# Kernel tuning notes

Hardware: AMD Instinct MI355X
Metric: run time of the kernel (lower is better)

The kernel has to match this reference:

```python
import jax, jax.numpy as jnp
import numpy as np

N = 50000
E = 800000
IN_DIM = 128
HEADS = 4
OUT_DIM = 32
TOT = HEADS * OUT_DIM  # 128 == IN_DIM -> residual_proj is None
LN_EPS = 1e-5
NEG_SLOPE = 0.2


def setup_inputs() -> dict:
    key = jax.random.key(0)
    ks = jax.random.split(key, 10)
    x = jax.random.normal(ks[0], (N, IN_DIM), dtype=jnp.float32)
    # random edges guaranteed src != dst (PyG GATv2Conv removes then re-adds self loops)
    src = jax.random.randint(ks[1], (E,), 0, N)
    off = jax.random.randint(ks[2], (E,), 1, N)
    dst = (src + off) % N
    edge_index = jnp.stack([src, dst]).astype(jnp.int64)
    # glorot-style init for weights
    sc = 1.0 / np.sqrt(IN_DIM)
    W_l = jax.random.uniform(ks[3], (IN_DIM, TOT), jnp.float32, -sc, sc)
    b_l = jnp.zeros((TOT,), jnp.float32)
    W_r = jax.random.uniform(ks[4], (IN_DIM, TOT), jnp.float32, -sc, sc)
    b_r = jnp.zeros((TOT,), jnp.float32)
    att = jax.random.uniform(ks[5], (HEADS, OUT_DIM), jnp.float32, -sc, sc)
    bias = jnp.zeros((TOT,), jnp.float32)
    ln_g = jnp.ones((TOT,), jnp.float32)
    ln_b = jnp.zeros((TOT,), jnp.float32)
    return {"x": x, "edge_index": edge_index, "W_l": W_l, "b_l": b_l,
            "W_r": W_r, "b_r": b_r, "att": att, "bias": bias,
            "ln_g": ln_g, "ln_b": ln_b}


def _gatv2_layer(x, src, dst, W_l, b_l, W_r, b_r, att, bias, ln_g, ln_b):
    n = x.shape[0]
    # GATv2Conv: x_l = lin_l(x) (source/messages), x_r = lin_r(x) (target)
    xl = (x @ W_l + b_l).reshape(n, HEADS, OUT_DIM)
    xr = (x @ W_r + b_r).reshape(n, HEADS, OUT_DIM)
    m = xl[src] + xr[dst]                               # [E+N, H, D]
    s = jnp.einsum('ehd,hd->eh', jax.nn.leaky_relu(m, NEG_SLOPE), att)
    # per-destination softmax (every node has a self loop -> no empty segments)
    smax = jax.ops.segment_max(s, dst, num_segments=n)  # [N, H]
    e = jnp.exp(s - smax[dst])
    denom = jax.ops.segment_sum(e, dst, num_segments=n)
    alpha = e / denom[dst]                              # [E+N, H]
    out = jax.ops.segment_sum(alpha[..., None] * xl[src], dst, num_segments=n)
    out = out.reshape(n, TOT) + bias
    out = out + x                                       # residual (in_dim == total_out_dim)
    mu = jnp.mean(out, axis=-1, keepdims=True)
    var = jnp.mean(jnp.square(out - mu), axis=-1, keepdims=True)
    y = (out - mu) / jnp.sqrt(var + LN_EPS) * ln_g + ln_b
    return jax.nn.elu(y)


def reference(x, edge_index, W_l, b_l, W_r, b_r, att, bias, ln_g, ln_b):
    n = x.shape[0]
    loops = jnp.arange(n, dtype=edge_index.dtype)
    src = jnp.concatenate([edge_index[0], loops])
    dst = jnp.concatenate([edge_index[1], loops])
    return _gatv2_layer(x, src, dst, W_l, b_l, W_r, b_r, att, bias, ln_g, ln_b)
```

## Files before the change

### kernel.cpp

```cpp
#include <hip/hip_runtime.h>

#define N_NODES 50000
#define E_EDGES 800000
#define M_TOTAL (E_EDGES + N_NODES)
#define IN_DIM 128
#define HEADS 4
#define OUT_DIM 32
#define TOT 128
#define LN_EPS 1e-5f
#define NEG_SLOPE 0.2f
#define LOG2E 1.4426950408889634f

#define SCAN_NBLK ((N_NODES + 255) / 256)
#define GEMM_NBLK ((N_NODES + 63) / 64)
#define HIST_NBLK 128
#define EPB 6656
#define HEPB (EPB / 2)
#define SCAT_NBLK (HIST_NBLK * 2)

typedef __bf16 bf16x8 __attribute__((ext_vector_type(8)));
typedef float  f32x4  __attribute__((ext_vector_type(4)));
typedef _Float16 h2   __attribute__((ext_vector_type(2)));

__device__ __forceinline__ float quad_sum(float p) {
    p += __int_as_float(__builtin_amdgcn_update_dpp(
        0, __float_as_int(p), 0xB1 , 0xF, 0xF, true));
    p += __int_as_float(__builtin_amdgcn_update_dpp(
        0, __float_as_int(p), 0x4E , 0xF, 0xF, true));
    return p;
}

__global__ __launch_bounds__(256) void wthist_kernel(
    const int* __restrict__ dsts,
    const float* __restrict__ Wl, const float* __restrict__ Wr,
    unsigned* __restrict__ WT, unsigned char* __restrict__ HP,
    unsigned char* __restrict__ rank8) {
    __shared__ unsigned cnt[N_NODES / 4];
    const int b = blockIdx.x, t = threadIdx.x;
    if (b < 64) {
        const int u = b * 256 + t;
        const int col = u >> 6, k2 = u & 63;
        const float* __restrict__ W = (col < 128) ? Wl : Wr;
        const int c = col & 127;
        union { __bf16 bb[2]; unsigned uu; } p;
        p.bb[0] = (__bf16)W[(2 * k2) * TOT + c];
        p.bb[1] = (__bf16)W[(2 * k2 + 1) * TOT + c];
        WT[col * 64 + k2] = p.uu;
        return;
    }
    const int hb = b - 64;
    const int m_begin = hb * EPB;
    const int m_end = min(m_begin + EPB, M_TOTAL);
    for (int i = t; i < N_NODES / 4; i += 256) cnt[i] = 0;
    __syncthreads();
    for (int m0 = m_begin + t * 4; m0 < m_end; m0 += 1024) {
        int d[4];
        if (m0 < E_EDGES) {
            const int4 dv = *(const int4*)&dsts[m0];
            d[0] = dv.x; d[1] = dv.y; d[2] = dv.z; d[3] = dv.w;
        } else {
            d[0] = m0 - E_EDGES; d[1] = d[0] + 1; d[2] = d[0] + 2; d[3] = d[0] + 3;
        }
        uchar4 r;
        unsigned old, sh;
        sh = (d[0] & 3) * 8; old = atomicAdd(&cnt[d[0] >> 2], 1u << sh);
        r.x = (unsigned char)(old >> sh);
        sh = (d[1] & 3) * 8; old = atomicAdd(&cnt[d[1] >> 2], 1u << sh);
        r.y = (unsigned char)(old >> sh);
        sh = (d[2] & 3) * 8; old = atomicAdd(&cnt[d[2] >> 2], 1u << sh);
        r.z = (unsigned char)(old >> sh);
        sh = (d[3] & 3) * 8; old = atomicAdd(&cnt[d[3] >> 2], 1u << sh);
        r.w = (unsigned char)(old >> sh);
        *(uchar4*)&rank8[m0] = r;
    }
    __syncthreads();
    unsigned* __restrict__ Hrow = (unsigned*)(HP + (size_t)hb * N_NODES);
    for (int i = t; i < N_NODES / 4; i += 256) Hrow[i] = cnt[i];
}

__global__ __launch_bounds__(256) void scan1gemm_kernel(
    unsigned char* __restrict__ HP,
    int* __restrict__ incl, int* __restrict__ blockSums,
    int* __restrict__ degtot,
    const float* __restrict__ x, const unsigned* __restrict__ WT,
    const float* __restrict__ bl, const float* __restrict__ br,
    unsigned* __restrict__ xlb, unsigned* __restrict__ xrb) {
    __shared__ float epi[4][16][66];
    const int t = threadIdx.x;
    if (blockIdx.x >= GEMM_NBLK) {
        int* sh = (int*)epi;
        const int i = (blockIdx.x - GEMM_NBLK) * 256 + t;
        int tot = 0;
        if (i < N_NODES) {
            int run = 0;
#pragma unroll 16
            for (int b = 0; b < HIST_NBLK; ++b) {
                const int h = HP[(size_t)b * N_NODES + i];
                HP[(size_t)b * N_NODES + i] = (unsigned char)run;
                run += h;
            }
            tot = run;
            degtot[i] = tot;
        }
        sh[t] = tot;
        __syncthreads();
#pragma unroll
        for (int off = 1; off < 256; off <<= 1) {
            int u = (t >= off) ? sh[t - off] : 0;
            __syncthreads();
            sh[t] += u;
            __syncthreads();
        }
        if (i < N_NODES) incl[i] = sh[t];
        if (t == 255) blockSums[blockIdx.x - GEMM_NBLK] = sh[255];
        return;
    }
    const int w = t >> 6, lane = t & 63;
    const int q = lane >> 4, ln = lane & 15;
    const int m0 = blockIdx.x * 64;

    const int row = min(m0 + w * 16 + ln, N_NODES - 1);
    const float* __restrict__ xrow = x + (size_t)row * IN_DIM;
    bf16x8 A[4];
#pragma unroll
    for (int c = 0; c < 4; ++c) {
        const float4 v0 = *(const float4*)&xrow[c * 32 + q * 8];
        const float4 v1 = *(const float4*)&xrow[c * 32 + q * 8 + 4];
        bf16x8 a;
        a[0] = (__bf16)v0.x; a[1] = (__bf16)v0.y; a[2] = (__bf16)v0.z; a[3] = (__bf16)v0.w;
        a[4] = (__bf16)v1.x; a[5] = (__bf16)v1.y; a[6] = (__bf16)v1.z; a[7] = (__bf16)v1.w;
        A[c] = a;
    }

    const int mr = lane >> 2, cg2 = (lane & 3) * 16;
    const int grow = m0 + w * 16 + mr;
#pragma unroll
    for (int g = 0; g < 4; ++g) {
        const int n0 = g * 64;
        const float* __restrict__ bvec = (g < 2) ? bl : br;
        f32x4 acc[4];
#pragma unroll
        for (int nt = 0; nt < 4; ++nt) {
            const float b = bvec[(n0 & 127) + nt * 16 + ln];
            acc[nt] = (f32x4){b, b, b, b};
        }
#pragma unroll
        for (int nt = 0; nt < 4; ++nt) {
            const int col = n0 + nt * 16 + ln;
#pragma unroll
            for (int c = 0; c < 4; ++c) {
                const bf16x8 B = *(const bf16x8*)&WT[col * 64 + c * 16 + q * 4];
                acc[nt] = __builtin_amdgcn_mfma_f32_16x16x32_bf16(A[c], B, acc[nt], 0, 0, 0);
            }
        }
#pragma unroll
        for (int nt = 0; nt < 4; ++nt)
#pragma unroll
            for (int r = 0; r < 4; ++r)
                epi[w][q * 4 + r][nt * 16 + ln] = acc[nt][r];

        if (grow < N_NODES) {
            unsigned p[8];
#pragma unroll
            for (int i = 0; i < 8; ++i) {
                union { _Float16 h[2]; unsigned u; } pk;
                pk.h[0] = (_Float16)epi[w][mr][cg2 + 2 * i];
                pk.h[1] = (_Float16)epi[w][mr][cg2 + 2 * i + 1];
                p[i] = pk.u;
            }
            unsigned* __restrict__ dst = ((g < 2) ? xlb : xrb) +
                (size_t)grow * 64 + (g & 1) * 32 + (cg2 >> 1);
            *(uint4*)&dst[0] = make_uint4(p[0], p[1], p[2], p[3]);
            *(uint4*)&dst[4] = make_uint4(p[4], p[5], p[6], p[7]);
        }
    }
}

__global__ __launch_bounds__(256) void scan23_kernel(
    const int* __restrict__ degtot, const int* __restrict__ blockSums,
    int* __restrict__ rowptr ,
    unsigned short* __restrict__ sorted16) {
    __shared__ int sh[256];
    const int t = threadIdx.x;
    const int v0 = (t < SCAN_NBLK) ? blockSums[t] : 0;
    sh[t] = v0;
    __syncthreads();
#pragma unroll
    for (int off = 1; off < 256; off <<= 1) {
        int u = (t >= off) ? sh[t - off] : 0;
        __syncthreads();
        sh[t] += u;
        __syncthreads();
    }
    const int blockOff = (blockIdx.x == 0) ? 0 : sh[blockIdx.x - 1];
    const int i = blockIdx.x * 256 + t;
    if (i < N_NODES)
        rowptr[i] = blockOff + rowptr[i] - degtot[i];
    if (i == 0) rowptr[N_NODES] = M_TOTAL;
    if (blockIdx.x == 0 && t < 32) sorted16[M_TOTAL + t] = 0;
}

__global__ __launch_bounds__(512) void scatter_kernel(
    const int* __restrict__ srcs, const int* __restrict__ dsts,
    const int* __restrict__ rowptr, const unsigned char* __restrict__ P,
    const unsigned char* __restrict__ rank8,
    unsigned short* __restrict__ sorted16) {
    __shared__ __align__(16) unsigned char smem[N_NODES];
    const int t = threadIdx.x;
    const int sb = blockIdx.x;
    const int hb = sb >> 1;
    const uint4* __restrict__ Prow = (const uint4*)(P + (size_t)hb * N_NODES);
    for (int i = t; i < N_NODES / 16; i += 512)
        ((uint4*)smem)[i] = Prow[i];
    __syncthreads();
    const int eb = hb * EPB + (sb & 1) * HEPB;
    const int ee = min(eb + HEPB, M_TOTAL);
    for (int m0 = eb + t * 4; m0 < ee; m0 += 2048) {
        int s[4], d[4];
        if (m0 < E_EDGES) {
            const int4 sv = *(const int4*)&srcs[m0];
            const int4 dv = *(const int4*)&dsts[m0];
            s[0] = sv.x; s[1] = sv.y; s[2] = sv.z; s[3] = sv.w;
            d[0] = dv.x; d[1] = dv.y; d[2] = dv.z; d[3] = dv.w;
        } else {
            s[0] = d[0] = m0 - E_EDGES;
            s[1] = d[1] = d[0] + 1; s[2] = d[2] = d[0] + 2; s[3] = d[3] = d[0] + 3;
        }
        const uchar4 r = *(const uchar4*)&rank8[m0];
        sorted16[rowptr[d[0]] + (int)smem[d[0]] + (int)r.x] = (unsigned short)s[0];
        sorted16[rowptr[d[1]] + (int)smem[d[1]] + (int)r.y] = (unsigned short)s[1];
        sorted16[rowptr[d[2]] + (int)smem[d[2]] + (int)r.z] = (unsigned short)s[2];
        sorted16[rowptr[d[3]] + (int)smem[d[3]] + (int)r.w] = (unsigned short)s[3];
    }
}

__global__ __launch_bounds__(256) void gat_kernel(
    const int* __restrict__ rowptr, const unsigned short* __restrict__ sorted16,
    const unsigned* __restrict__ xlb, const unsigned* __restrict__ xrb,
    const float* __restrict__ att, const float* __restrict__ x,
    const float* __restrict__ bias, const float* __restrict__ g,
    const float* __restrict__ bvec, float* __restrict__ out) {
    const int d = blockIdx.x * 4 + (threadIdx.x >> 6);
    const int lane = threadIdx.x & 63;
    const int ln = lane & 15, q = lane >> 4;
    if (d >= N_NODES) return;

    h2 xrh[4], ath[4];
    {
        const uint4 ur = *(const uint4*)&xrb[(size_t)d * 64 + 4 * ln];
        union { uint4 u; h2 h[4]; } cr; cr.u = ur;
        xrh[0] = cr.h[0]; xrh[1] = cr.h[1]; xrh[2] = cr.h[2]; xrh[3] = cr.h[3];
        const float4 a0 = *(const float4*)&att[8 * ln];
        const float4 a1 = *(const float4*)&att[8 * ln + 4];
        ath[0][0] = (_Float16)(a0.x * LOG2E); ath[0][1] = (_Float16)(a0.y * LOG2E);
        ath[1][0] = (_Float16)(a0.z * LOG2E); ath[1][1] = (_Float16)(a0.w * LOG2E);
        ath[2][0] = (_Float16)(a1.x * LOG2E); ath[2][1] = (_Float16)(a1.y * LOG2E);
        ath[3][0] = (_Float16)(a1.z * LOG2E); ath[3][1] = (_Float16)(a1.w * LOG2E);
    }
    const h2 slope = (h2){(_Float16)NEG_SLOPE, (_Float16)NEG_SLOPE};
    const int beg = rowptr[d], end = rowptr[d + 1];

    float l = 0.f;
    h2 acc4[4];
#pragma unroll
    for (int k = 0; k < 4; ++k) acc4[k] = (h2){(_Float16)0.f, (_Float16)0.f};

    uint4 u0, u1;
    {
        const int sA0 = (int)sorted16[beg + q];
        const int sA1 = (int)sorted16[beg + 4 + q];
        u0 = *(const uint4*)&xlb[(size_t)sA0 * 64 + 4 * ln];
        u1 = *(const uint4*)&xlb[(size_t)sA1 * 64 + 4 * ln];
    }
    int sB0 = (int)sorted16[beg + 8 + q];
    int sB1 = (int)sorted16[beg + 12 + q];

    for (int base = beg; base < end; base += 8) {
        const int sC0 = (int)sorted16[base + 16 + q];
        const int sC1 = (int)sorted16[base + 20 + q];
        const uint4 un0 = *(const uint4*)&xlb[(size_t)sB0 * 64 + 4 * ln];
        const uint4 un1 = *(const uint4*)&xlb[(size_t)sB1 * 64 + 4 * ln];

        union { unsigned uu; h2 h; } a0, a1, a2, a3, b0, b1, b2, b3;
        a0.uu = u0.x; a1.uu = u0.y; a2.uu = u0.z; a3.uu = u0.w;
        b0.uu = u1.x; b1.uu = u1.y; b2.uu = u1.z; b3.uu = u1.w;
        h2 mA0 = a0.h + xrh[0], mA1 = a1.h + xrh[1];
        h2 mA2 = a2.h + xrh[2], mA3 = a3.h + xrh[3];
        h2 mB0 = b0.h + xrh[0], mB1 = b1.h + xrh[1];
        h2 mB2 = b2.h + xrh[2], mB3 = b3.h + xrh[3];
        mA0 = __builtin_elementwise_max(mA0, mA0 * slope);
        mA1 = __builtin_elementwise_max(mA1, mA1 * slope);
        mA2 = __builtin_elementwise_max(mA2, mA2 * slope);
        mA3 = __builtin_elementwise_max(mA3, mA3 * slope);
        mB0 = __builtin_elementwise_max(mB0, mB0 * slope);
        mB1 = __builtin_elementwise_max(mB1, mB1 * slope);
        mB2 = __builtin_elementwise_max(mB2, mB2 * slope);
        mB3 = __builtin_elementwise_max(mB3, mB3 * slope);
        float p0 = __builtin_amdgcn_fdot2(mA0, ath[0], 0.0f, false);
        p0 = __builtin_amdgcn_fdot2(mA1, ath[1], p0, false);
        p0 = __builtin_amdgcn_fdot2(mA2, ath[2], p0, false);
        p0 = __builtin_amdgcn_fdot2(mA3, ath[3], p0, false);
        float p1 = __builtin_amdgcn_fdot2(mB0, ath[0], 0.0f, false);
        p1 = __builtin_amdgcn_fdot2(mB1, ath[1], p1, false);
        p1 = __builtin_amdgcn_fdot2(mB2, ath[2], p1, false);
        p1 = __builtin_amdgcn_fdot2(mB3, ath[3], p1, false);
        p0 = quad_sum(p0);
        p1 = quad_sum(p1);
        const float e0 = (base + q < end) ? exp2f(p0) : 0.f;
        const float e1 = (base + 4 + q < end) ? exp2f(p1) : 0.f;
        l += e0 + e1;
        const _Float16 eh0 = (_Float16)e0, eh1 = (_Float16)e1;
        const h2 e20 = (h2){eh0, eh0}, e21 = (h2){eh1, eh1};
        acc4[0] += e20 * a0.h; acc4[0] += e21 * b0.h;
        acc4[1] += e20 * a1.h; acc4[1] += e21 * b1.h;
        acc4[2] += e20 * a2.h; acc4[2] += e21 * b2.h;
        acc4[3] += e20 * a3.h; acc4[3] += e21 * b3.h;

        u0 = un0; u1 = un1; sB0 = sC0; sB1 = sC1;
    }

#pragma unroll
    for (int off = 16; off <= 32; off <<= 1) {
        l += __shfl_xor(l, off, 64);
#pragma unroll
        for (int k = 0; k < 4; ++k) {
            union { h2 h; int i; } tmp; tmp.h = acc4[k];
            tmp.i = __shfl_xor(tmp.i, off, 64);
            acc4[k] += tmp.h;
        }
    }
    float acc[8];
#pragma unroll
    for (int k = 0; k < 4; ++k) {
        acc[2 * k]     = (float)acc4[k][0];
        acc[2 * k + 1] = (float)acc4[k][1];
    }

    const float inv_l = 1.0f / l;
    const float4 xv0 = *(const float4*)&x[(size_t)d * TOT + 8 * ln];
    const float4 xv1 = *(const float4*)&x[(size_t)d * TOT + 8 * ln + 4];
    const float4 bi0 = *(const float4*)&bias[8 * ln];
    const float4 bi1 = *(const float4*)&bias[8 * ln + 4];
    float v[8];
    v[0] = fmaf(acc[0], inv_l, bi0.x + xv0.x);
    v[1] = fmaf(acc[1], inv_l, bi0.y + xv0.y);
    v[2] = fmaf(acc[2], inv_l, bi0.z + xv0.z);
    v[3] = fmaf(acc[3], inv_l, bi0.w + xv0.w);
    v[4] = fmaf(acc[4], inv_l, bi1.x + xv1.x);
    v[5] = fmaf(acc[5], inv_l, bi1.y + xv1.y);
    v[6] = fmaf(acc[6], inv_l, bi1.z + xv1.z);
    v[7] = fmaf(acc[7], inv_l, bi1.w + xv1.w);
    float sum = 0.f, sq = 0.f;
#pragma unroll
    for (int k = 0; k < 8; ++k) { sum += v[k]; sq = fmaf(v[k], v[k], sq); }
#pragma unroll
    for (int off = 1; off <= 8; off <<= 1) {
        sum += __shfl_xor(sum, off, 64);
        sq  += __shfl_xor(sq,  off, 64);
    }
    const float mu  = sum * (1.0f / TOT);
    const float var = sq * (1.0f / TOT) - mu * mu;
    const float inv = rsqrtf(var + LN_EPS);
    const float4 g0 = *(const float4*)&g[8 * ln];
    const float4 g1 = *(const float4*)&g[8 * ln + 4];
    const float4 b0 = *(const float4*)&bvec[8 * ln];
    const float4 b1 = *(const float4*)&bvec[8 * ln + 4];
    float y[8];
    y[0] = (v[0] - mu) * inv * g0.x + b0.x;
    y[1] = (v[1] - mu) * inv * g0.y + b0.y;
    y[2] = (v[2] - mu) * inv * g0.z + b0.z;
    y[3] = (v[3] - mu) * inv * g0.w + b0.w;
    y[4] = (v[4] - mu) * inv * g1.x + b1.x;
    y[5] = (v[5] - mu) * inv * g1.y + b1.y;
    y[6] = (v[6] - mu) * inv * g1.z + b1.z;
    y[7] = (v[7] - mu) * inv * g1.w + b1.w;
#pragma unroll
    for (int k = 0; k < 8; ++k) y[k] = y[k] > 0.f ? y[k] : __expf(y[k]) - 1.f;
    if (q < 2) {
        float4 o = (q == 0) ? make_float4(y[0], y[1], y[2], y[3])
                            : make_float4(y[4], y[5], y[6], y[7]);
        *(float4*)&out[(size_t)d * TOT + 8 * ln + 4 * q] = o;
    }
}

extern "C" void kernel_launch(void* const* d_in, const int* in_sizes, int n_in,
                              void* d_out, int out_size, void* d_ws, size_t ws_size,
                              hipStream_t stream) {
    const float* x    = (const float*)d_in[0];
    const int*   ei   = (const int*)d_in[1];
    const float* Wl   = (const float*)d_in[2];
    const float* bl   = (const float*)d_in[3];
    const float* Wr   = (const float*)d_in[4];
    const float* br   = (const float*)d_in[5];
    const float* att  = (const float*)d_in[6];
    const float* bias = (const float*)d_in[7];
    const float* ln_g = (const float*)d_in[8];
    const float* ln_b = (const float*)d_in[9];
    const int* srcs = ei;
    const int* dsts = ei + E_EDGES;

    unsigned* xlb = (unsigned*)d_ws;
    unsigned* xrb = xlb + (size_t)N_NODES * 64;
    int*   degtot     = (int*)(xrb + (size_t)N_NODES * 64);
    int*   rowptr     = degtot + N_NODES;
    int*   blockSums  = rowptr + N_NODES + 1;
    unsigned* WT      = (unsigned*)(blockSums + SCAN_NBLK + 3);
    unsigned char* HP = (unsigned char*)(WT + 256 * 64);
    unsigned short* sorted16 = (unsigned short*)(HP + (size_t)HIST_NBLK * N_NODES);
    unsigned char*  rank8    = (unsigned char*)(sorted16 + M_TOTAL + 32);

    wthist_kernel<<<64 + HIST_NBLK, 256, 0, stream>>>(dsts, Wl, Wr, WT, HP, rank8);
    scan1gemm_kernel<<<GEMM_NBLK + SCAN_NBLK, 256, 0, stream>>>(
        HP, rowptr, blockSums, degtot, x, WT, bl, br, xlb, xrb);
    scan23_kernel<<<SCAN_NBLK, 256, 0, stream>>>(degtot, blockSums, rowptr, sorted16);
    scatter_kernel<<<SCAT_NBLK, 512, 0, stream>>>(srcs, dsts, rowptr, HP, rank8, sorted16);
    gat_kernel<<<(N_NODES + 3) / 4, 256, 0, stream>>>(rowptr, sorted16, xlb, xrb, att, x,
                                                      bias, ln_g, ln_b, (float*)d_out);
}
```

Measured before the change: 188.6 us.

## Split GEMM and scan kernels, stage weights in LDS, widen scatter blocks

The fused scan/GEMM kernel is split into separate GEMM and scan1 launches. The GEMM now stages each 64-column weight slice in shared memory before the MFMA loop instead of reading it from global memory per lane. The scatter kernel goes from two 512-thread blocks per histogram row to one 1024-thread block, so each histogram row is loaded into LDS once rather than twice. The gat kernel clamps its prefetch indices to the segment end. The split adds a kernel launch and loses the overlap between scan and GEMM work, and the larger scatter blocks halve the number of blocks in flight.

Result: faster. 175.3 us (-7.1%).

```diff
diff --git a/kernel.cpp b/kernel.cpp
--- a/kernel.cpp
+++ b/kernel.cpp
@@ -15,8 +15,6 @@
 #define GEMM_NBLK ((N_NODES + 63) / 64)
 #define HIST_NBLK 128
 #define EPB 6656
-#define HEPB (EPB / 2)
-#define SCAT_NBLK (HIST_NBLK * 2)
 
 typedef __bf16 bf16x8 __attribute__((ext_vector_type(8)));
 typedef float  f32x4  __attribute__((ext_vector_type(4)));
@@ -78,44 +76,13 @@
     for (int i = t; i < N_NODES / 4; i += 256) Hrow[i] = cnt[i];
 }
 
-__global__ __launch_bounds__(256) void scan1gemm_kernel(
-    unsigned char* __restrict__ HP,
-    int* __restrict__ incl, int* __restrict__ blockSums,
-    int* __restrict__ degtot,
+__global__ __launch_bounds__(256) void gemm_kernel(
     const float* __restrict__ x, const unsigned* __restrict__ WT,
     const float* __restrict__ bl, const float* __restrict__ br,
     unsigned* __restrict__ xlb, unsigned* __restrict__ xrb) {
     __shared__ float epi[4][16][66];
-    const int t = threadIdx.x;
-    if (blockIdx.x >= GEMM_NBLK) {
-        int* sh = (int*)epi;
-        const int i = (blockIdx.x - GEMM_NBLK) * 256 + t;
-        int tot = 0;
-        if (i < N_NODES) {
-            int run = 0;
-#pragma unroll 16
-            for (int b = 0; b < HIST_NBLK; ++b) {
-                const int h = HP[(size_t)b * N_NODES + i];
-                HP[(size_t)b * N_NODES + i] = (unsigned char)run;
-                run += h;
-            }
-            tot = run;
-            degtot[i] = tot;
-        }
-        sh[t] = tot;
-        __syncthreads();
-#pragma unroll
-        for (int off = 1; off < 256; off <<= 1) {
-            int u = (t >= off) ? sh[t - off] : 0;
-            __syncthreads();
-            sh[t] += u;
-            __syncthreads();
-        }
-        if (i < N_NODES) incl[i] = sh[t];
-        if (t == 255) blockSums[blockIdx.x - GEMM_NBLK] = sh[255];
-        return;
-    }
-    const int w = t >> 6, lane = t & 63;
+    __shared__ unsigned Bs[64][68];
+    const int t = threadIdx.x, w = t >> 6, lane = t & 63;
     const int q = lane >> 4, ln = lane & 15;
     const int m0 = blockIdx.x * 64;
 
@@ -137,6 +104,17 @@
 #pragma unroll
     for (int g = 0; g < 4; ++g) {
         const int n0 = g * 64;
+        __syncthreads();
+        {
+            const unsigned* __restrict__ src = WT + n0 * 64;
+#pragma unroll
+            for (int it = 0; it < 4; ++it) {
+                const int dw = t * 4 + it * 1024;
+                const uint4 v = *(const uint4*)&src[dw];
+                *(uint4*)&Bs[dw >> 6][dw & 63] = v;
+            }
+        }
+        __syncthreads();
         const float* __restrict__ bvec = (g < 2) ? bl : br;
         f32x4 acc[4];
 #pragma unroll
@@ -146,10 +124,9 @@
         }
 #pragma unroll
         for (int nt = 0; nt < 4; ++nt) {
-            const int col = n0 + nt * 16 + ln;
 #pragma unroll
             for (int c = 0; c < 4; ++c) {
-                const bf16x8 B = *(const bf16x8*)&WT[col * 64 + c * 16 + q * 4];
+                const bf16x8 B = *(const bf16x8*)&Bs[nt * 16 + ln][c * 16 + q * 4];
                 acc[nt] = __builtin_amdgcn_mfma_f32_16x16x32_bf16(A[c], B, acc[nt], 0, 0, 0);
             }
         }
@@ -176,6 +153,38 @@
     }
 }
 
+__global__ __launch_bounds__(256) void scan1_kernel(
+    unsigned char* __restrict__ HP,
+    int* __restrict__ incl, int* __restrict__ blockSums,
+    int* __restrict__ degtot) {
+    __shared__ int sh[256];
+    const int t = threadIdx.x;
+    const int i = blockIdx.x * 256 + t;
+    int tot = 0;
+    if (i < N_NODES) {
+        int run = 0;
+#pragma unroll 16
+        for (int b = 0; b < HIST_NBLK; ++b) {
+            const int h = HP[(size_t)b * N_NODES + i];
+            HP[(size_t)b * N_NODES + i] = (unsigned char)run;
+            run += h;
+        }
+        tot = run;
+        degtot[i] = tot;
+    }
+    sh[t] = tot;
+    __syncthreads();
+#pragma unroll
+    for (int off = 1; off < 256; off <<= 1) {
+        int u = (t >= off) ? sh[t - off] : 0;
+        __syncthreads();
+        sh[t] += u;
+        __syncthreads();
+    }
+    if (i < N_NODES) incl[i] = sh[t];
+    if (t == 255) blockSums[blockIdx.x] = sh[255];
+}
+
 __global__ __launch_bounds__(256) void scan23_kernel(
     const int* __restrict__ degtot, const int* __restrict__ blockSums,
     int* __restrict__ rowptr ,
@@ -200,22 +209,21 @@
     if (blockIdx.x == 0 && t < 32) sorted16[M_TOTAL + t] = 0;
 }
 
-__global__ __launch_bounds__(512) void scatter_kernel(
+__global__ __launch_bounds__(1024) void scatter_kernel(
     const int* __restrict__ srcs, const int* __restrict__ dsts,
     const int* __restrict__ rowptr, const unsigned char* __restrict__ P,
     const unsigned char* __restrict__ rank8,
     unsigned short* __restrict__ sorted16) {
     __shared__ __align__(16) unsigned char smem[N_NODES];
     const int t = threadIdx.x;
-    const int sb = blockIdx.x;
-    const int hb = sb >> 1;
+    const int hb = blockIdx.x;
     const uint4* __restrict__ Prow = (const uint4*)(P + (size_t)hb * N_NODES);
-    for (int i = t; i < N_NODES / 16; i += 512)
+    for (int i = t; i < N_NODES / 16; i += 1024)
         ((uint4*)smem)[i] = Prow[i];
     __syncthreads();
-    const int eb = hb * EPB + (sb & 1) * HEPB;
-    const int ee = min(eb + HEPB, M_TOTAL);
-    for (int m0 = eb + t * 4; m0 < ee; m0 += 2048) {
+    const int eb = hb * EPB;
+    const int ee = min(eb + EPB, M_TOTAL);
+    for (int m0 = eb + t * 4; m0 < ee; m0 += 4096) {
         int s[4], d[4];
         if (m0 < E_EDGES) {
             const int4 sv = *(const int4*)&srcs[m0];
@@ -267,17 +275,17 @@
 
     uint4 u0, u1;
     {
-        const int sA0 = (int)sorted16[beg + q];
-        const int sA1 = (int)sorted16[beg + 4 + q];
+        const int sA0 = (int)sorted16[min(beg + q, end - 1)];
+        const int sA1 = (int)sorted16[min(beg + 4 + q, end - 1)];
         u0 = *(const uint4*)&xlb[(size_t)sA0 * 64 + 4 * ln];
         u1 = *(const uint4*)&xlb[(size_t)sA1 * 64 + 4 * ln];
     }
-    int sB0 = (int)sorted16[beg + 8 + q];
-    int sB1 = (int)sorted16[beg + 12 + q];
+    int sB0 = (int)sorted16[min(beg + 8 + q, end - 1)];
+    int sB1 = (int)sorted16[min(beg + 12 + q, end - 1)];
 
     for (int base = beg; base < end; base += 8) {
-        const int sC0 = (int)sorted16[base + 16 + q];
-        const int sC1 = (int)sorted16[base + 20 + q];
+        const int sC0 = (int)sorted16[min(base + 16 + q, end - 1)];
+        const int sC1 = (int)sorted16[min(base + 20 + q, end - 1)];
         const uint4 un0 = *(const uint4*)&xlb[(size_t)sB0 * 64 + 4 * ln];
         const uint4 un1 = *(const uint4*)&xlb[(size_t)sB1 * 64 + 4 * ln];
 
@@ -410,10 +418,10 @@
     unsigned char*  rank8    = (unsigned char*)(sorted16 + M_TOTAL + 32);
 
     wthist_kernel<<<64 + HIST_NBLK, 256, 0, stream>>>(dsts, Wl, Wr, WT, HP, rank8);
-    scan1gemm_kernel<<<GEMM_NBLK + SCAN_NBLK, 256, 0, stream>>>(
-        HP, rowptr, blockSums, degtot, x, WT, bl, br, xlb, xrb);
+    gemm_kernel<<<GEMM_NBLK, 256, 0, stream>>>(x, WT, bl, br, xlb, xrb);
+    scan1_kernel<<<SCAN_NBLK, 256, 0, stream>>>(HP, rowptr, blockSums, degtot);
     scan23_kernel<<<SCAN_NBLK, 256, 0, stream>>>(degtot, blockSums, rowptr, sorted16);
-    scatter_kernel<<<SCAT_NBLK, 512, 0, stream>>>(srcs, dsts, rowptr, HP, rank8, sorted16);
+    scatter_kernel<<<HIST_NBLK, 1024, 0, stream>>>(srcs, dsts, rowptr, HP, rank8, sorted16);
     gat_kernel<<<(N_NODES + 3) / 4, 256, 0, stream>>>(rowptr, sorted16, xlb, xrb, att, x,
                                                       bias, ln_g, ln_b, (float*)d_out);
 }
```
